# Kernel optimization log

Hardware: AMD Instinct MI355X
Metric: run time of the kernel (lower is better)

Reference implementation:

```python
import math
import jax, jax.numpy as jnp
import numpy as np

B, T, F, H, DK = 64, 128, 512, 8, 64
L, R = 128, 128
W = L + T + R           # 384 attention window per chunk
P = 2 * T - 1 + L + R   # 511 relative position length


def setup_inputs() -> dict:
    key = jax.random.key(0)
    ks = jax.random.split(key, 16)
    s = 0.02
    return {
        "query": jax.random.normal(ks[0], (B, T, F), jnp.float32),
        "key": jax.random.normal(ks[1], (B, T, F), jnp.float32),
        "value": jax.random.normal(ks[2], (B, T, F), jnp.float32),
        "mask": jnp.ones((B, 1, W), dtype=bool),
        "pos_emb": jax.random.normal(ks[3], (1, P, F), jnp.float32),
        "cache": jax.random.normal(ks[4], (L, H, 2 * DK), jnp.float32),
        "W_q": jax.random.normal(ks[5], (F, F), jnp.float32) * s,
        "b_q": jnp.zeros((F,), jnp.float32),
        "W_k": jax.random.normal(ks[6], (F, F), jnp.float32) * s,
        "b_k": jnp.zeros((F,), jnp.float32),
        "W_v": jax.random.normal(ks[7], (F, F), jnp.float32) * s,
        "b_v": jnp.zeros((F,), jnp.float32),
        "W_pos": jax.random.normal(ks[8], (F, F), jnp.float32) * s,
        "pos_bias_u": jax.random.normal(ks[9], (H, DK), jnp.float32) * s,
        "pos_bias_v": jax.random.normal(ks[10], (H, DK), jnp.float32) * s,
        "W_out": jax.random.normal(ks[11], (F, F), jnp.float32) * s,
        "b_out": jnp.zeros((F,), jnp.float32),
        "right_context_size": R,
        "left_context_size": L,
        "truncated_context_size": B * T,
    }


def reference(query, key, value, mask, pos_emb, cache,
              W_q, b_q, W_k, b_k, W_v, b_v, W_pos,
              pos_bias_u, pos_bias_v, W_out, b_out,
              right_context_size, left_context_size, truncated_context_size):
    b, t, f = query.shape
    h, d_k = pos_bias_u.shape
    # QKV projections -> (B, T, h, d_k)
    q = (query @ W_q + b_q).reshape(b, t, h, d_k)
    k = (key @ W_k + b_k).reshape(b, t, h, d_k)
    v = (value @ W_v + b_v).reshape(b, t, h, d_k)
    # flatten chunks to one long stream of kv pairs, prepend left-context cache
    kv = jnp.concatenate([k, v], axis=-1).reshape(b * t, h, 2 * d_k)
    kv = jnp.concatenate([cache, kv], axis=0)  # (L + B*T, h, 2d)
    Lc = cache.shape[0]
    new_cache = kv[:truncated_context_size + Lc][-Lc:]  # (L, h, 2d)
    kv = jnp.pad(kv, ((0, right_context_size), (0, 0), (0, 0)))
    win = Lc + t + right_context_size
    idx = jnp.arange(b)[:, None] * t + jnp.arange(win)[None, :]
    kv_win = jnp.transpose(kv[idx], (0, 2, 1, 3))
    k_w, v_w = kv_win[..., :d_k], kv_win[..., d_k:]
    # relative position projection -> (h, P, d_k)
    p = (pos_emb @ W_pos).reshape(pos_emb.shape[0], -1, h, d_k)
    p = jnp.transpose(p, (0, 2, 1, 3))[0]
    q_u = jnp.transpose(q + pos_bias_u, (0, 2, 1, 3))  # (B, h, T, d)
    q_v = jnp.transpose(q + pos_bias_v, (0, 2, 1, 3))
    matrix_ac = jnp.einsum('bhtd,bhwd->bhtw', q_u, k_w)
    matrix_bd = jnp.einsum('bhtd,hpd->bhtp', q_v, p)      # (B,h,T,P)
    # rel_shift: out[..., i, j] = bd[..., i, (T-1) - i + j]
    shift = (t - 1) - jnp.arange(t)[:, None] + jnp.arange(win)[None, :]
    matrix_bd = jnp.take_along_axis(matrix_bd, shift[None, None], axis=-1)
    scores = (matrix_ac + matrix_bd) / math.sqrt(d_k)
    if mask.shape[2] > 0:
        neg = ~mask[:, None, :, :win]
        scores = jnp.where(neg, -jnp.inf, scores)
        attn = jax.nn.softmax(scores, axis=-1)
        attn = jnp.where(neg, 0.0, attn)
    else:
        attn = jax.nn.softmax(scores, axis=-1)
    x = jnp.einsum('bhtw,bhwd->bhtd', attn, v_w)  # (B,h,T,d)
    x = jnp.transpose(x, (0, 2, 1, 3)).reshape(b, t, h * d_k)
    out = x @ W_out + b_out
    return out, new_cache
```

## Files before the change

### kernel.cpp

```cpp
#include <hip/hip_runtime.h>

typedef __attribute__((ext_vector_type(8))) __bf16 bf16x8;
typedef __attribute__((ext_vector_type(4))) float f32x4;
typedef __attribute__((ext_vector_type(8))) unsigned short ushort8;

#define LDST 88
#define GEXT 8448

__device__ __forceinline__ unsigned short f2bf(float x) {
  unsigned int u = __float_as_uint(x);
  return (unsigned short)((u + 0x7FFFu + ((u >> 16) & 1u)) >> 16);
}
__device__ __forceinline__ float bf2f(unsigned short b) {
  return __uint_as_float(((unsigned int)b) << 16);
}
__device__ __forceinline__ f32x4 mfma16(ushort8 a, ushort8 b, f32x4 c) {
  return __builtin_amdgcn_mfma_f32_16x16x32_bf16(
      __builtin_bit_cast(bf16x8, a), __builtin_bit_cast(bf16x8, b), c, 0, 0, 0);
}
__device__ __forceinline__ unsigned int cvtpk(float lo, float hi) {
  unsigned int r;
  asm("v_cvt_pk_bf16_f32 %0, %1, %2" : "=v"(r) : "v"(lo), "v"(hi));
  return r;
}
__device__ __forceinline__ void gload16(const unsigned short* g, unsigned short* l) {
  __builtin_amdgcn_global_load_lds(
      (const __attribute__((address_space(1))) unsigned int*)g,
      (__attribute__((address_space(3))) unsigned int*)l, 16, 0, 0);
}
__device__ __forceinline__ ushort8 addbias(ushort8 a, const float* __restrict__ bias,
                                           int dbase) {
  ushort8 o;
#pragma unroll
  for (int j = 0; j < 8; ++j) o[j] = f2bf(bf2f(a[j]) + bias[dbase + j] * 0.125f);
  return o;
}

__global__ __launch_bounds__(256) void prep_all(
    const float* __restrict__ wq, const float* __restrict__ wk,
    const float* __restrict__ wv, const float* __restrict__ wpos,
    const float* __restrict__ wout, unsigned short* __restrict__ WtBase,
    const float* __restrict__ q, const float* __restrict__ k,
    const float* __restrict__ v, const float* __restrict__ pos,
    unsigned short* __restrict__ Qb, unsigned short* __restrict__ Kb,
    unsigned short* __restrict__ Vb, unsigned short* __restrict__ Pb,
    const float* __restrict__ cache, unsigned short* __restrict__ Kx,
    unsigned short* __restrict__ Vt) {
  __shared__ unsigned short lds[64][LDST];
  const int bid = blockIdx.x;
  if (bid < 320) {
    const int z = bid >> 6, rem = bid & 63;
    const float* W;
    switch (z) {
      case 0: W = wq; break;
      case 1: W = wk; break;
      case 2: W = wv; break;
      case 3: W = wpos; break;
      default: W = wout; break;
    }
    unsigned short* Wt = WtBase + (long)z * 262144;
    const int n0 = (rem & 7) * 64, k0 = (rem >> 3) * 64;
    const int row = threadIdx.x >> 3;
    const int cc = (threadIdx.x & 7) * 8;
#pragma unroll
    for (int p = 0; p < 2; ++p) {
      int kk = row + p * 32;
      const float* s = W + (long)(k0 + kk) * 512 + n0 + cc;
      float4 f0 = *(const float4*)s;
      float4 f1 = *(const float4*)(s + 4);
      ushort8 vv;
      vv[0] = f2bf(f0.x); vv[1] = f2bf(f0.y); vv[2] = f2bf(f0.z); vv[3] = f2bf(f0.w);
      vv[4] = f2bf(f1.x); vv[5] = f2bf(f1.y); vv[6] = f2bf(f1.z); vv[7] = f2bf(f1.w);
      *(ushort8*)&lds[kk][cc] = vv;
    }
    __syncthreads();
#pragma unroll
    for (int p = 0; p < 2; ++p) {
      int n = row + p * 32;
      ushort8 o;
#pragma unroll
      for (int j = 0; j < 8; ++j) o[j] = lds[cc + j][n];
      *(ushort8*)(Wt + (long)(n0 + n) * 512 + k0 + cc) = o;
    }
  } else if (bid < 6592) {
    long u = (long)(bid - 320) * 256 + threadIdx.x;
    const float* src;
    unsigned short* dst;
    long off;
    bool z = false;
    if (u < 524288) { src = q; dst = Qb; off = u; }
    else if (u < 1048576) { src = k; dst = Kb; off = u - 524288; }
    else if (u < 1572864) { src = v; dst = Vb; off = u - 1048576; }
    else { src = pos; dst = Pb; off = u - 1572864; z = (off >= 32704); }
    uint4 w = uint4{0u, 0u, 0u, 0u};
    if (!z) {
      float4 f0 = *(const float4*)(src + off * 8);
      float4 f1 = *(const float4*)(src + off * 8 + 4);
      w.x = cvtpk(f0.x, f0.y);
      w.y = cvtpk(f0.z, f0.w);
      w.z = cvtpk(f1.x, f1.y);
      w.w = cvtpk(f1.z, f1.w);
    }
    *(uint4*)(dst + off * 8) = w;
  } else {
    int i = (bid - 6592) * 256 + threadIdx.x;
    int d = i & 63, g = (i >> 6) & 127, h = i >> 13;
    float kv = cache[(long)(g * 8 + h) * 128 + d];
    float vv = cache[(long)(g * 8 + h) * 128 + 64 + d];
    Kx[((long)h * GEXT + g) * 64 + d] = f2bf(kv);
    Kx[((long)h * GEXT + 8320 + g) * 64 + d] = 0;
    Vt[((long)(h * 64 + d)) * GEXT + g] = f2bf(vv);
    Vt[((long)(h * 64 + d)) * GEXT + 8320 + g] = 0;
  }
}

__device__ __forceinline__ void mainloop_sb(const unsigned short* __restrict__ A,
                                            int m0,
                                            const unsigned short* __restrict__ Wt,
                                            int n0, unsigned short* __restrict__ Alds,
                                            unsigned short* __restrict__ Blds,
                                            f32x4 (&acc)[4][4]) {
  const int tid = threadIdx.x;
  const int lane = tid & 63;
  const int wid = tid >> 6;
  const int wr = wid >> 1, wc = wid & 1;
  const int sperm = ((lane & 7) ^ ((lane >> 3) & 7)) * 8;
#pragma unroll 1
  for (int t = 0; t < 8; ++t) {
    const int k0 = t * 64;
#pragma unroll
    for (int i = 0; i < 4; ++i) {
      const int c = wid * 4 + i;
      gload16(A + (long)(m0 + c * 8 + (lane >> 3)) * 512 + k0 + sperm,
              Alds + c * 512);
      gload16(Wt + (long)(n0 + c * 8 + (lane >> 3)) * 512 + k0 + sperm,
              Blds + c * 512);
    }
    __syncthreads();
#pragma unroll
    for (int kk = 0; kk < 2; ++kk) {
      const int slot = (kk * 4 + (lane >> 4)) ^ (lane & 7);
      ushort8 af[4], bf[4];
#pragma unroll
      for (int mt = 0; mt < 4; ++mt) {
        const int arow = wr * 64 + mt * 16 + (lane & 15);
        af[mt] = *(const ushort8*)&Alds[arow * 64 + slot * 8];
      }
#pragma unroll
      for (int nt = 0; nt < 4; ++nt) {
        const int brow = wc * 64 + nt * 16 + (lane & 15);
        bf[nt] = *(const ushort8*)&Blds[brow * 64 + slot * 8];
      }
#pragma unroll
      for (int mt = 0; mt < 4; ++mt)
#pragma unroll
        for (int nt = 0; nt < 4; ++nt)
          acc[mt][nt] = mfma16(af[mt], bf[nt], acc[mt][nt]);
    }
    __syncthreads();
  }
}

__device__ __forceinline__ void mainloop_2c32(const unsigned short* __restrict__ A,
                                              int m0,
                                              const unsigned short* __restrict__ Wt,
                                              int n0, unsigned short* __restrict__ AldsB,
                                              unsigned short* __restrict__ BldsB,
                                              f32x4 (&acc)[4][4]) {
  const int tid = threadIdx.x;
  const int lane = tid & 63;
  const int wid = tid >> 6;
  const int wr = wid >> 1, wc = wid & 1;
  const int q4 = lane >> 4;
  const int ln15 = lane & 15;
  const int srow = tid >> 2;
  const int sperm = (((tid & 3) ^ ((tid >> 3) & 3)) << 3);
#define STG32(k0, Ab, Bb)                                                        \
  {                                                                              \
    _Pragma("unroll") for (int i = 0; i < 2; ++i) {                              \
      const int row_ = i * 64 + srow;                                            \
      gload16(A + (long)(m0 + row_) * 512 + (k0) + sperm,                        \
              (Ab) + i * 2048 + wid * 512);                                      \
      gload16(Wt + (long)(n0 + row_) * 512 + (k0) + sperm,                       \
              (Bb) + i * 2048 + wid * 512);                                      \
    }                                                                            \
  }
  STG32(0, AldsB, BldsB);
  asm volatile("s_waitcnt vmcnt(0)" ::: "memory");
  __builtin_amdgcn_s_barrier();
  __builtin_amdgcn_sched_barrier(0);
#pragma unroll
  for (int t = 0; t < 16; ++t) {
    const int cur = t & 1;
    unsigned short* Ac = AldsB + cur * 4096;
    unsigned short* Bc = BldsB + cur * 4096;
    if (t < 15) {
      STG32((t + 1) * 32, AldsB + (cur ^ 1) * 4096, BldsB + (cur ^ 1) * 4096);
      asm volatile("s_waitcnt vmcnt(4)" ::: "memory");
    } else {
      asm volatile("s_waitcnt vmcnt(0)" ::: "memory");
    }
    __builtin_amdgcn_s_barrier();
    __builtin_amdgcn_sched_barrier(0);
    ushort8 af[4], bf[4];
#pragma unroll
    for (int mt = 0; mt < 4; ++mt) {
      const int arow = wr * 64 + mt * 16 + ln15;
      af[mt] = *(const ushort8*)&Ac[arow * 32 + ((q4 ^ ((arow >> 1) & 3)) << 3)];
    }
#pragma unroll
    for (int nt = 0; nt < 4; ++nt) {
      const int brow = wc * 64 + nt * 16 + ln15;
      bf[nt] = *(const ushort8*)&Bc[brow * 32 + ((q4 ^ ((brow >> 1) & 3)) << 3)];
    }
#pragma unroll
    for (int mt = 0; mt < 4; ++mt)
#pragma unroll
      for (int nt = 0; nt < 4; ++nt)
        acc[mt][nt] = mfma16(af[mt], bf[nt], acc[mt][nt]);
    __builtin_amdgcn_s_barrier();
    __builtin_amdgcn_sched_barrier(0);
  }
#undef STG32
}

__global__ __launch_bounds__(256) void gemm_qkv128(
    const unsigned short* __restrict__ Qb, const unsigned short* __restrict__ Kb2,
    const unsigned short* __restrict__ Vb2, const unsigned short* __restrict__ WtQ,
    const unsigned short* __restrict__ WtK, const unsigned short* __restrict__ WtV,
    const float* __restrict__ bq, const float* __restrict__ bk,
    const float* __restrict__ bv, unsigned short* __restrict__ Qp,
    unsigned short* __restrict__ Kx, unsigned short* __restrict__ Vt,
    float* __restrict__ cache_out) {
  __shared__ unsigned short S[16384];
  unsigned short* AldsB = S;
  unsigned short* BldsB = S + 8192;
  const int tid = threadIdx.x;
  const int w = (blockIdx.x & 7) * 96 + (blockIdx.x >> 3);
  const int type = w >> 8;
  const int rem = w & 255;
  const int m0 = (rem >> 2) * 128;
  const int n0 = (rem & 3) * 128;
  const int h_base = n0 >> 6;
  const unsigned short* A = type == 0 ? Qb : (type == 1 ? Kb2 : Vb2);
  const unsigned short* Wt = type == 0 ? WtQ : (type == 1 ? WtK : WtV);
  const float* bias = type == 0 ? bq : (type == 1 ? bk : bv);
  f32x4 acc[4][4];
#pragma unroll
  for (int i = 0; i < 4; ++i)
#pragma unroll
    for (int j = 0; j < 4; ++j) acc[i][j] = f32x4{0.f, 0.f, 0.f, 0.f};
  mainloop_2c32(A, m0, Wt, n0, AldsB, BldsB, acc);
  __syncthreads();
  const int lane = tid & 63;
  const int wid = tid >> 6;
  const int wr = wid >> 1, wc = wid & 1;
  const int q4 = lane >> 4;
  const int ln15 = lane & 15;
  unsigned short* T = S;

  if (type == 0) {
#pragma unroll
    for (int mt = 0; mt < 4; ++mt)
#pragma unroll
      for (int nt = 0; nt < 4; ++nt)
#pragma unroll
        for (int r = 0; r < 4; ++r) {
          const int rl = wr * 64 + mt * 16 + q4 * 4 + r;
          const int cl = wc * 64 + nt * 16 + ln15;
          const int gcol = n0 + cl;
          const float val = acc[mt][nt][r] + bias[gcol];
          T[rl * 128 + ((((cl >> 3) ^ (rl & 15)) << 3) | (cl & 7))] =
              f2bf(val * 0.125f);
        }
    __syncthreads();
    {
      const int hl = tid >> 7, rr = tid & 127;
      unsigned short* dst = Qp + ((long)(h_base + hl) * 8192 + m0 + rr) * 64;
#pragma unroll
      for (int j = 0; j < 8; ++j) {
        const int g = (hl * 8 + j) ^ (rr & 15);
        *(ushort8*)(dst + j * 8) = *(const ushort8*)&T[rr * 128 + g * 8];
      }
    }
  } else if (type == 1) {
#pragma unroll
    for (int mt = 0; mt < 4; ++mt)
#pragma unroll
      for (int nt = 0; nt < 4; ++nt)
#pragma unroll
        for (int r = 0; r < 4; ++r) {
          const int rl = wr * 64 + mt * 16 + q4 * 4 + r;
          const int cl = wc * 64 + nt * 16 + ln15;
          const int gcol = n0 + cl;
          const float val = acc[mt][nt][r] + bias[gcol];
          const int grow = m0 + rl;
          if (grow >= 8064)
            cache_out[(long)(grow - 8064) * 1024 + (gcol >> 6) * 128 + (gcol & 63)] = val;
          T[rl * 128 + ((((cl >> 3) ^ (rl & 15)) << 3) | (cl & 7))] = f2bf(val);
        }
    __syncthreads();
    {
      const int hl = tid >> 7, rr = tid & 127;
      unsigned short* dst = Kx + ((long)(h_base + hl) * GEXT + 128 + m0 + rr) * 64;
#pragma unroll
      for (int j = 0; j < 8; ++j) {
        const int g = (hl * 8 + j) ^ (rr & 15);
        *(ushort8*)(dst + j * 8) = *(const ushort8*)&T[rr * 128 + g * 8];
      }
    }
  } else {
#pragma unroll
    for (int mt = 0; mt < 4; ++mt)
#pragma unroll
      for (int nt = 0; nt < 4; ++nt)
#pragma unroll
        for (int r = 0; r < 4; ++r) {
          const int rl = wr * 64 + mt * 16 + q4 * 4 + r;
          const int cl = wc * 64 + nt * 16 + ln15;
          const int gcol = n0 + cl;
          const float val = acc[mt][nt][r] + bias[gcol];
          const int grow = m0 + rl;
          if (grow >= 8064)
            cache_out[(long)(grow - 8064) * 1024 + (gcol >> 6) * 128 + 64 + (gcol & 63)] = val;
          T[cl * 128 + ((((rl >> 3) ^ (cl & 15)) << 3) | (rl & 7))] = f2bf(val);
        }
    __syncthreads();
    {
      const int dl = tid >> 1, half = tid & 1;
      unsigned short* dst = Vt +
          ((long)(h_base + (dl >> 6)) * 64 + (dl & 63)) * GEXT + 128 + m0 + half * 64;
#pragma unroll
      for (int j = 0; j < 8; ++j) {
        const int g = (half * 8 + j) ^ (dl & 15);
        *(ushort8*)(dst + j * 8) = *(const ushort8*)&T[dl * 128 + g * 8];
      }
    }
  }
}

__global__ __launch_bounds__(256) void gemm_pos128(const unsigned short* __restrict__ Posb,
                                                   const unsigned short* __restrict__ WtP,
                                                   unsigned short* __restrict__ Pm) {
  __shared__ unsigned short Alds[8192];
  __shared__ unsigned short Blds[8192];
  const int m0 = (blockIdx.x >> 2) * 128;
  const int n0 = (blockIdx.x & 3) * 128;
  f32x4 acc[4][4];
#pragma unroll
  for (int i = 0; i < 4; ++i)
#pragma unroll
    for (int j = 0; j < 4; ++j) acc[i][j] = f32x4{0.f, 0.f, 0.f, 0.f};
  mainloop_sb(Posb, m0, WtP, n0, Alds, Blds, acc);
  const int lane = threadIdx.x & 63;
  const int wid = threadIdx.x >> 6;
  const int wr = wid >> 1, wc = wid & 1;
#pragma unroll
  for (int mt = 0; mt < 4; ++mt)
#pragma unroll
    for (int nt = 0; nt < 4; ++nt)
#pragma unroll
      for (int r = 0; r < 4; ++r) {
        const int grow = m0 + wr * 64 + mt * 16 + (lane >> 4) * 4 + r;
        const int gcol = n0 + wc * 64 + nt * 16 + (lane & 15);
        const int h = gcol >> 6, d = gcol & 63;
        Pm[((long)h * 512 + grow) * 64 + d] = f2bf(acc[mt][nt][r]);
      }
}

__global__ __launch_bounds__(256) void gemm_out128(const unsigned short* __restrict__ Xo,
                                                   const unsigned short* __restrict__ WtO,
                                                   const float* __restrict__ bout,
                                                   float* __restrict__ out) {
  __shared__ unsigned short Alds[8192];
  __shared__ unsigned short Blds[8192];
  const int w = (blockIdx.x & 7) * 32 + (blockIdx.x >> 3);
  const int m0 = (w >> 2) * 128;
  const int n0 = (w & 3) * 128;
  f32x4 acc[4][4];
#pragma unroll
  for (int i = 0; i < 4; ++i)
#pragma unroll
    for (int j = 0; j < 4; ++j) acc[i][j] = f32x4{0.f, 0.f, 0.f, 0.f};
  mainloop_2c32(Xo, m0, WtO, n0, Alds, Blds, acc);
  const int lane = threadIdx.x & 63;
  const int wid = threadIdx.x >> 6;
  const int wr = wid >> 1, wc = wid & 1;
#pragma unroll
  for (int mt = 0; mt < 4; ++mt)
#pragma unroll
    for (int nt = 0; nt < 4; ++nt)
#pragma unroll
      for (int r = 0; r < 4; ++r) {
        const int grow = m0 + wr * 64 + mt * 16 + (lane >> 4) * 4 + r;
        const int gcol = n0 + wc * 64 + nt * 16 + (lane & 15);
        out[(long)grow * 512 + gcol] = acc[mt][nt][r] + bout[gcol];
      }
}

__global__ __launch_bounds__(256) void bd_kernel(const unsigned short* __restrict__ Qp,
                                                 const float* __restrict__ bvv,
                                                 const unsigned short* __restrict__ Pm,
                                                 unsigned short* __restrict__ BDs) {
  __shared__ unsigned short Pc[2][8192];
  const int bh = blockIdx.x;
  const int b = bh >> 3, h = bh & 7;
  const int lane = threadIdx.x & 63;
  const int wave = threadIdx.x >> 6;
  const int q4 = lane >> 4;
  const int ln15 = lane & 15;
  const int t0 = wave * 32;
  const int sperm = ((lane & 7) ^ ((lane >> 3) & 7)) * 8;
  const unsigned short* Pmh = Pm + (long)h * 512 * 64;

#define STAGE_P(c, p)                                                            \
  {                                                                              \
    _Pragma("unroll") for (int i = 0; i < 4; ++i) {                              \
      gload16(Pmh + (long)((c) * 128 + i * 32 + wave * 8 + (lane >> 3)) * 64 +   \
                  sperm,                                                         \
              &Pc[p][(i * 32 + wave * 8) * 64]);                                 \
    }                                                                            \
  }

  ushort8 qf[2][2];
#pragma unroll
  for (int mt = 0; mt < 2; ++mt)
#pragma unroll
    for (int kk = 0; kk < 2; ++kk) {
      ushort8 raw = *(const ushort8*)(Qp +
          ((long)h * 8192 + b * 128 + t0 + mt * 16 + ln15) * 64 +
          kk * 32 + q4 * 8);
      qf[mt][kk] = addbias(raw, bvv, h * 64 + kk * 32 + q4 * 8);
    }

  STAGE_P(0, 0);
  asm volatile("s_waitcnt vmcnt(0)" ::: "memory");
  __builtin_amdgcn_s_barrier();
  __builtin_amdgcn_sched_barrier(0);

#pragma unroll
  for (int c = 0; c < 4; ++c) {
    const int p = c & 1;
    if (c < 3) {
      STAGE_P(c + 1, p ^ 1);
      asm volatile("s_waitcnt vmcnt(4)" ::: "memory");
    } else {
      asm volatile("s_waitcnt vmcnt(0)" ::: "memory");
    }
    __builtin_amdgcn_s_barrier();
    __builtin_amdgcn_sched_barrier(0);
    f32x4 acc[2][8];
#pragma unroll
    for (int i = 0; i < 2; ++i)
#pragma unroll
      for (int j = 0; j < 8; ++j) acc[i][j] = f32x4{0.f, 0.f, 0.f, 0.f};
#pragma unroll
    for (int kk = 0; kk < 2; ++kk) {
#pragma unroll
      for (int nt = 0; nt < 8; ++nt) {
        ushort8 pf = *(const ushort8*)&Pc[p][(nt * 16 + ln15) * 64 +
                                            (((kk * 4 + q4) ^ (ln15 & 7)) * 8)];
        acc[0][nt] = mfma16(qf[0][kk], pf, acc[0][nt]);
        acc[1][nt] = mfma16(qf[1][kk], pf, acc[1][nt]);
      }
    }
#pragma unroll
    for (int mt = 0; mt < 2; ++mt)
#pragma unroll
      for (int nt = 0; nt < 8; ++nt)
#pragma unroll
        for (int r = 0; r < 4; ++r) {
          const int t = t0 + mt * 16 + q4 * 4 + r;
          const int pp = c * 128 + nt * 16 + ln15;
          const int w = pp - 127 + t;
          if (w >= 0 && w < 384)
            BDs[((long)bh * 128 + t) * 384 + w] = f2bf(acc[mt][nt][r]);
        }
    __builtin_amdgcn_s_barrier();
    __builtin_amdgcn_sched_barrier(0);
  }
#undef STAGE_P
}

__global__ __launch_bounds__(256) void attn_stage(
    const unsigned short* __restrict__ Qp, const float* __restrict__ bu,
    const unsigned short* __restrict__ BDs, const unsigned short* __restrict__ Kext,
    const unsigned short* __restrict__ Vtext, unsigned short* __restrict__ Xo) {
  __shared__ unsigned short Kc[2][4096];
  __shared__ unsigned short Vc[2][4096];
  __shared__ unsigned short Bc[4][1024];
  const int wsw = (blockIdx.x & 7) * 128 + (blockIdx.x >> 3);
  const int h = wsw >> 7;
  const int rem = wsw & 127;
  const int b = rem >> 1;
  const int thalf = rem & 1;
  const int lane = threadIdx.x & 63;
  const int wave = threadIdx.x >> 6;
  const int q4 = lane >> 4;
  const int ln15 = lane & 15;
  const int t0 = thalf * 64 + wave * 16;
  const long g0 = (long)b * 128;
  const int sperm = ((lane & 7) ^ ((lane >> 3) & 7)) * 8;
  const int rgran = (ln15 & 7);

  const unsigned short* Kb = Kext + (long)h * GEXT * 64;
  const unsigned short* Vb = Vtext + (long)h * 64 * GEXT;
  const unsigned short* Bd = BDs + ((long)(b * 8 + h) * 128 + t0) * 384;

#define STAGE_KV(cc, p)                                                          \
  {                                                                              \
    _Pragma("unroll") for (int i = 0; i < 2; ++i) {                              \
      const int row_ = wave * 16 + i * 8 + (lane >> 3);                          \
      gload16(Kb + (g0 + (cc) * 64 + row_) * 64 + sperm,                         \
              &Kc[p][(wave * 16 + i * 8) * 64]);                                 \
      gload16(Vb + (long)row_ * GEXT + g0 + (cc) * 64 + sperm,                   \
              &Vc[p][(wave * 16 + i * 8) * 64]);                                 \
    }                                                                            \
  }

#define STAGE_BD(cc)                                                             \
  {                                                                              \
    _Pragma("unroll") for (int i = 0; i < 2; ++i) {                              \
      const int row_ = i * 8 + (lane >> 3);                                      \
      gload16(Bd + (long)row_ * 384 + (cc) * 64 + sperm, &Bc[wave][i * 512]);    \
    }                                                                            \
  }

  ushort8 quf[2];
#pragma unroll
  for (int kk = 0; kk < 2; ++kk) {
    ushort8 raw = *(const ushort8*)(Qp +
        ((long)h * 8192 + b * 128 + t0 + ln15) * 64 + kk * 32 + q4 * 8);
    quf[kk] = addbias(raw, bu, h * 64 + kk * 32 + q4 * 8);
  }

  f32x4 acc2[4];
  float lsum[4] = {0.f, 0.f, 0.f, 0.f};
#pragma unroll
  for (int j = 0; j < 4; ++j) acc2[j] = f32x4{0.f, 0.f, 0.f, 0.f};

  STAGE_KV(0, 0);
  STAGE_BD(0);
  asm volatile("s_waitcnt vmcnt(0)" ::: "memory");
  __builtin_amdgcn_s_barrier();
  __builtin_amdgcn_sched_barrier(0);

#pragma unroll
  for (int c = 0; c < 6; ++c) {
    const int p = c & 1;
    if (c < 5) {
      STAGE_KV(c + 1, p ^ 1);
      asm volatile("s_waitcnt vmcnt(4)" ::: "memory");
    } else {
      asm volatile("s_waitcnt vmcnt(0)" ::: "memory");
    }
    __builtin_amdgcn_s_barrier();
    __builtin_amdgcn_sched_barrier(0);

    f32x4 acc[4];
#pragma unroll
    for (int nt = 0; nt < 4; ++nt) acc[nt] = f32x4{0.f, 0.f, 0.f, 0.f};
    __builtin_amdgcn_s_setprio(1);
#pragma unroll
    for (int kk = 0; kk < 2; ++kk)
#pragma unroll
      for (int nt = 0; nt < 4; ++nt) {
        ushort8 kf = *(const ushort8*)&Kc[p][(nt * 16 + ln15) * 64 +
                                            (((kk * 4 + q4) ^ rgran) * 8)];
        acc[nt] = mfma16(quf[kk], kf, acc[nt]);
      }
    __builtin_amdgcn_s_setprio(0);

#pragma unroll
    for (int nt = 0; nt < 4; ++nt)
#pragma unroll
      for (int r = 0; r < 4; ++r) {
        const int tl = q4 * 4 + r;
        const int g = (nt * 2 + (ln15 >> 3)) ^ (tl & 7);
        const int addr = tl * 64 + g * 8 + (ln15 & 7);
        const float s = acc[nt][r] + bf2f(Bc[wave][addr]);
        const float pv = exp2f(s * 1.4426950408889634f);
        lsum[r] += pv;
        Bc[wave][addr] = f2bf(pv);
      }

    __builtin_amdgcn_s_setprio(1);
#pragma unroll
    for (int kt = 0; kt < 2; ++kt) {
      ushort8 a = *(const ushort8*)&Bc[wave][ln15 * 64 + ((kt * 4 + q4) ^ rgran) * 8];
#pragma unroll
      for (int ntd = 0; ntd < 4; ++ntd) {
        ushort8 vf = *(const ushort8*)&Vc[p][(ntd * 16 + ln15) * 64 +
                                            (((kt * 4 + q4) ^ rgran) * 8)];
        acc2[ntd] = mfma16(a, vf, acc2[ntd]);
      }
    }
    __builtin_amdgcn_s_setprio(0);

    __builtin_amdgcn_sched_barrier(0);
    if (c < 5) STAGE_BD(c + 1);

    __builtin_amdgcn_s_barrier();
    __builtin_amdgcn_sched_barrier(0);
  }
#undef STAGE_KV
#undef STAGE_BD

#pragma unroll
  for (int r = 0; r < 4; ++r) {
    float s = lsum[r];
    s += __shfl_xor(s, 1);
    s += __shfl_xor(s, 2);
    s += __shfl_xor(s, 4);
    s += __shfl_xor(s, 8);
    const float rs = 1.0f / s;
    const int tl = t0 + q4 * 4 + r;
#pragma unroll
    for (int ntd = 0; ntd < 4; ++ntd) {
      const int dl = ntd * 16 + ln15;
      Xo[((long)b * 128 + tl) * 512 + h * 64 + dl] = f2bf(acc2[ntd][r] * rs);
    }
  }
}

extern "C" void kernel_launch(void* const* d_in, const int* in_sizes, int n_in,
                              void* d_out, int out_size, void* d_ws, size_t ws_size,
                              hipStream_t stream) {
  const float* query = (const float*)d_in[0];
  const float* key = (const float*)d_in[1];
  const float* value = (const float*)d_in[2];
  const float* pos = (const float*)d_in[4];
  const float* cache = (const float*)d_in[5];
  const float* Wq = (const float*)d_in[6];
  const float* bq = (const float*)d_in[7];
  const float* Wk = (const float*)d_in[8];
  const float* bk = (const float*)d_in[9];
  const float* Wv = (const float*)d_in[10];
  const float* bv = (const float*)d_in[11];
  const float* Wpos = (const float*)d_in[12];
  const float* bu = (const float*)d_in[13];
  const float* bvv = (const float*)d_in[14];
  const float* Wout = (const float*)d_in[15];
  const float* bout = (const float*)d_in[16];

  float* out = (float*)d_out;
  float* cache_out = out + 4194304;

  unsigned short* ws = (unsigned short*)d_ws;
  unsigned short* WtQ = ws;
  unsigned short* WtK = WtQ + 262144;
  unsigned short* WtV = WtK + 262144;
  unsigned short* WtP = WtV + 262144;
  unsigned short* WtO = WtP + 262144;
  unsigned short* Pm  = WtO + 262144;
  unsigned short* Qp  = Pm + 262144;
  unsigned short* Qv  = Qp + 4194304;
  unsigned short* Kx  = Qv + 4194304;
  unsigned short* Vx  = Kx + 4325376;
  unsigned short* Vt  = Vx + 4325376;
  unsigned short* Xo  = Vt + 4325376;
  unsigned short* Qb  = Xo + 4194304;
  unsigned short* Kb2 = Qb + 4194304;
  unsigned short* Vb2 = Kb2 + 4194304;
  unsigned short* Posb = Vb2 + 4194304;
  unsigned short* BDs = Qb;

  prep_all<<<6848, 256, 0, stream>>>(Wq, Wk, Wv, Wpos, Wout, WtQ,
                                     query, key, value, pos, Qb, Kb2, Vb2, Posb,
                                     cache, Kx, Vt);
  gemm_qkv128<<<768, 256, 0, stream>>>(Qb, Kb2, Vb2, WtQ, WtK, WtV,
                                       bq, bk, bv, Qp, Kx, Vt, cache_out);
  gemm_pos128<<<16, 256, 0, stream>>>(Posb, WtP, Pm);
  bd_kernel<<<512, 256, 0, stream>>>(Qp, bvv, Pm, BDs);
  attn_stage<<<1024, 256, 0, stream>>>(Qp, bu, BDs, Kx, Vt, Xo);
  gemm_out128<<<256, 256, 0, stream>>>(Xo, WtO, bout, out);
}
```

Measured before the change: 117.4 us.

## Fuse fp32-to-bf16 activation conversion into QKV GEMM mainloop

Removes the separate pass in prep_all that converts the query/key/value activations to bf16. The QKV GEMM now streams fp32 A tiles directly into LDS via global_load_lds and converts them to bf16 with v_cvt_pk when building MFMA fragments. This avoids writing and re-reading a bf16 copy of the activations (about 24MB of extra traffic). In exchange the A tiles double in size, LDS use rises from 32KB to 48KB per block, and each tile is converted again for every N-tile that reads it.

```diff
diff --git a/kernel.cpp b/kernel.cpp
--- a/kernel.cpp
+++ b/kernel.cpp
@@ -28,6 +28,11 @@
       (const __attribute__((address_space(1))) unsigned int*)g,
       (__attribute__((address_space(3))) unsigned int*)l, 16, 0, 0);
 }
+__device__ __forceinline__ void gload16f(const float* g, unsigned short* l) {
+  __builtin_amdgcn_global_load_lds(
+      (const __attribute__((address_space(1))) unsigned int*)g,
+      (__attribute__((address_space(3))) unsigned int*)l, 16, 0, 0);
+}
 __device__ __forceinline__ ushort8 addbias(ushort8 a, const float* __restrict__ bias,
                                            int dbase) {
   ushort8 o;
@@ -40,10 +45,7 @@
     const float* __restrict__ wq, const float* __restrict__ wk,
     const float* __restrict__ wv, const float* __restrict__ wpos,
     const float* __restrict__ wout, unsigned short* __restrict__ WtBase,
-    const float* __restrict__ q, const float* __restrict__ k,
-    const float* __restrict__ v, const float* __restrict__ pos,
-    unsigned short* __restrict__ Qb, unsigned short* __restrict__ Kb,
-    unsigned short* __restrict__ Vb, unsigned short* __restrict__ Pb,
+    const float* __restrict__ pos, unsigned short* __restrict__ Pb,
     const float* __restrict__ cache, unsigned short* __restrict__ Kx,
     unsigned short* __restrict__ Vt) {
   __shared__ unsigned short lds[64][LDST];
@@ -82,28 +84,20 @@
       for (int j = 0; j < 8; ++j) o[j] = lds[cc + j][n];
       *(ushort8*)(Wt + (long)(n0 + n) * 512 + k0 + cc) = o;
     }
-  } else if (bid < 6592) {
-    long u = (long)(bid - 320) * 256 + threadIdx.x;
-    const float* src;
-    unsigned short* dst;
-    long off;
-    bool z = false;
-    if (u < 524288) { src = q; dst = Qb; off = u; }
-    else if (u < 1048576) { src = k; dst = Kb; off = u - 524288; }
-    else if (u < 1572864) { src = v; dst = Vb; off = u - 1048576; }
-    else { src = pos; dst = Pb; off = u - 1572864; z = (off >= 32704); }
+  } else if (bid < 448) {
+    long off = (long)(bid - 320) * 256 + threadIdx.x;
     uint4 w = uint4{0u, 0u, 0u, 0u};
-    if (!z) {
-      float4 f0 = *(const float4*)(src + off * 8);
-      float4 f1 = *(const float4*)(src + off * 8 + 4);
+    if (off < 32704) {
+      float4 f0 = *(const float4*)(pos + off * 8);
+      float4 f1 = *(const float4*)(pos + off * 8 + 4);
       w.x = cvtpk(f0.x, f0.y);
       w.y = cvtpk(f0.z, f0.w);
       w.z = cvtpk(f1.x, f1.y);
       w.w = cvtpk(f1.z, f1.w);
     }
-    *(uint4*)(dst + off * 8) = w;
+    *(uint4*)(Pb + off * 8) = w;
   } else {
-    int i = (bid - 6592) * 256 + threadIdx.x;
+    int i = (bid - 448) * 256 + threadIdx.x;
     int d = i & 63, g = (i >> 6) & 127, h = i >> 13;
     float kv = cache[(long)(g * 8 + h) * 128 + d];
     float vv = cache[(long)(g * 8 + h) * 128 + 64 + d];
@@ -224,17 +218,94 @@
 #undef STG32
 }
 
+__device__ __forceinline__ void mainloop_f32a(const float* __restrict__ A,
+                                              int m0,
+                                              const unsigned short* __restrict__ Wt,
+                                              int n0, unsigned short* __restrict__ AldsB,
+                                              unsigned short* __restrict__ BldsB,
+                                              f32x4 (&acc)[4][4]) {
+  const int tid = threadIdx.x;
+  const int lane = tid & 63;
+  const int wid = tid >> 6;
+  const int wr = wid >> 1, wc = wid & 1;
+  const int q4 = lane >> 4;
+  const int ln15 = lane & 15;
+  const int srow = tid >> 2;
+  const int sperm = (((tid & 3) ^ ((tid >> 3) & 3)) << 3);
+  const int arow_s = lane >> 3;
+  const int agr = lane & 7;
+#define STGF(k0, Ab, Bb)                                                         \
+  {                                                                              \
+    _Pragma("unroll") for (int i = 0; i < 4; ++i) {                              \
+      const int row_ = i * 32 + wid * 8 + arow_s;                                \
+      const int sp_ = ((((agr >> 1) ^ (row_ & 3)) << 1) | (agr & 1));            \
+      gload16f(A + (long)(m0 + row_) * 512 + (k0) + sp_ * 4,                     \
+               (Ab) + (i * 32 + wid * 8) * 64);                                  \
+    }                                                                            \
+    _Pragma("unroll") for (int i = 0; i < 2; ++i) {                              \
+      const int row_ = i * 64 + srow;                                            \
+      gload16(Wt + (long)(n0 + row_) * 512 + (k0) + sperm,                       \
+              (Bb) + i * 2048 + wid * 512);                                      \
+    }                                                                            \
+  }
+  STGF(0, AldsB, BldsB);
+  asm volatile("s_waitcnt vmcnt(0)" ::: "memory");
+  __builtin_amdgcn_s_barrier();
+  __builtin_amdgcn_sched_barrier(0);
+#pragma unroll
+  for (int t = 0; t < 16; ++t) {
+    const int cur = t & 1;
+    const float* Af = (const float*)(AldsB + cur * 8192);
+    unsigned short* Bc = BldsB + cur * 4096;
+    if (t < 15) {
+      STGF((t + 1) * 32, AldsB + (cur ^ 1) * 8192, BldsB + (cur ^ 1) * 4096);
+      asm volatile("s_waitcnt vmcnt(6)" ::: "memory");
+    } else {
+      asm volatile("s_waitcnt vmcnt(0)" ::: "memory");
+    }
+    __builtin_amdgcn_s_barrier();
+    __builtin_amdgcn_sched_barrier(0);
+    ushort8 af[4], bf[4];
+#pragma unroll
+    for (int mt = 0; mt < 4; ++mt) {
+      const int arow = wr * 64 + mt * 16 + ln15;
+      const int pr = q4 ^ (arow & 3);
+      const float4 f0 = *(const float4*)(Af + arow * 32 + pr * 8);
+      const float4 f1 = *(const float4*)(Af + arow * 32 + pr * 8 + 4);
+      uint4 u;
+      u.x = cvtpk(f0.x, f0.y);
+      u.y = cvtpk(f0.z, f0.w);
+      u.z = cvtpk(f1.x, f1.y);
+      u.w = cvtpk(f1.z, f1.w);
+      af[mt] = __builtin_bit_cast(ushort8, u);
+    }
+#pragma unroll
+    for (int nt = 0; nt < 4; ++nt) {
+      const int brow = wc * 64 + nt * 16 + ln15;
+      bf[nt] = *(const ushort8*)&Bc[brow * 32 + ((q4 ^ ((brow >> 1) & 3)) << 3)];
+    }
+#pragma unroll
+    for (int mt = 0; mt < 4; ++mt)
+#pragma unroll
+      for (int nt = 0; nt < 4; ++nt)
+        acc[mt][nt] = mfma16(af[mt], bf[nt], acc[mt][nt]);
+    __builtin_amdgcn_s_barrier();
+    __builtin_amdgcn_sched_barrier(0);
+  }
+#undef STGF
+}
+
 __global__ __launch_bounds__(256) void gemm_qkv128(
-    const unsigned short* __restrict__ Qb, const unsigned short* __restrict__ Kb2,
-    const unsigned short* __restrict__ Vb2, const unsigned short* __restrict__ WtQ,
+    const float* __restrict__ qin, const float* __restrict__ kin,
+    const float* __restrict__ vin, const unsigned short* __restrict__ WtQ,
     const unsigned short* __restrict__ WtK, const unsigned short* __restrict__ WtV,
     const float* __restrict__ bq, const float* __restrict__ bk,
     const float* __restrict__ bv, unsigned short* __restrict__ Qp,
     unsigned short* __restrict__ Kx, unsigned short* __restrict__ Vt,
     float* __restrict__ cache_out) {
-  __shared__ unsigned short S[16384];
+  __shared__ unsigned short S[24576];
   unsigned short* AldsB = S;
-  unsigned short* BldsB = S + 8192;
+  unsigned short* BldsB = S + 16384;
   const int tid = threadIdx.x;
   const int w = (blockIdx.x & 7) * 96 + (blockIdx.x >> 3);
   const int type = w >> 8;
@@ -242,7 +313,7 @@
   const int m0 = (rem >> 2) * 128;
   const int n0 = (rem & 3) * 128;
   const int h_base = n0 >> 6;
-  const unsigned short* A = type == 0 ? Qb : (type == 1 ? Kb2 : Vb2);
+  const float* A = type == 0 ? qin : (type == 1 ? kin : vin);
   const unsigned short* Wt = type == 0 ? WtQ : (type == 1 ? WtK : WtV);
   const float* bias = type == 0 ? bq : (type == 1 ? bk : bv);
   f32x4 acc[4][4];
@@ -250,7 +321,7 @@
   for (int i = 0; i < 4; ++i)
 #pragma unroll
     for (int j = 0; j < 4; ++j) acc[i][j] = f32x4{0.f, 0.f, 0.f, 0.f};
-  mainloop_2c32(A, m0, Wt, n0, AldsB, BldsB, acc);
+  mainloop_f32a(A, m0, Wt, n0, AldsB, BldsB, acc);
   __syncthreads();
   const int lane = tid & 63;
   const int wid = tid >> 6;
@@ -660,15 +731,12 @@
   unsigned short* Vt  = Vx + 4325376;
   unsigned short* Xo  = Vt + 4325376;
   unsigned short* Qb  = Xo + 4194304;
-  unsigned short* Kb2 = Qb + 4194304;
-  unsigned short* Vb2 = Kb2 + 4194304;
-  unsigned short* Posb = Vb2 + 4194304;
+  unsigned short* Posb = Qb + 3 * 4194304;
   unsigned short* BDs = Qb;
 
-  prep_all<<<6848, 256, 0, stream>>>(Wq, Wk, Wv, Wpos, Wout, WtQ,
-                                     query, key, value, pos, Qb, Kb2, Vb2, Posb,
-                                     cache, Kx, Vt);
-  gemm_qkv128<<<768, 256, 0, stream>>>(Qb, Kb2, Vb2, WtQ, WtK, WtV,
+  prep_all<<<704, 256, 0, stream>>>(Wq, Wk, Wv, Wpos, Wout, WtQ,
+                                    pos, Posb, cache, Kx, Vt);
+  gemm_qkv128<<<768, 256, 0, stream>>>(query, key, value, WtQ, WtK, WtV,
                                        bq, bk, bv, Qp, Kx, Vt, cache_out);
   gemm_pos128<<<16, 256, 0, stream>>>(Posb, WtP, Pm);
   bd_kernel<<<512, 256, 0, stream>>>(Qp, bvv, Pm, BDs);
```

After: 110.4 us. 1.06x faster.
